# Optimization experiments

Hardware: AMD Instinct MI355X
Metric: run time of the kernel (lower is better)

## Reference

```python
import jax, jax.numpy as jnp
import numpy as np

B, IN, FS, S, H = 4096, 4096, 4096, 64, 512  # batch, input_size, first_size, shape_lstm, n_hidden
D = FS // S  # per-step feature for left/right (=64); up/down per-step feature = S (=64)


def _lstm_cell(x, h, c, Wih, Whh, bih, bhh):
    # standard torch LSTMCell gate order: i, f, g, o
    g = x @ Wih.T + bih + h @ Whh.T + bhh  # (B, 4H)
    i, f, gg, o = jnp.split(g, 4, axis=-1)
    c = jax.nn.sigmoid(f) * c + jax.nn.sigmoid(i) * jnp.tanh(gg)
    h = jax.nn.sigmoid(o) * jnp.tanh(c)
    return h, c


def setup_inputs() -> dict:
    key = jax.random.key(0)
    ks = jax.random.split(key, 20)
    def cell(k, d_in):
        k1, k2, k3, k4 = jax.random.split(k, 4)
        s = 1.0 / np.sqrt(H)
        return (jax.random.uniform(k1, (4 * H, d_in), jnp.float32, -s, s),
                jax.random.uniform(k2, (4 * H, H), jnp.float32, -s, s),
                jax.random.uniform(k3, (4 * H,), jnp.float32, -s, s),
                jax.random.uniform(k4, (4 * H,), jnp.float32, -s, s))
    Wih_l, Whh_l, bih_l, bhh_l = cell(ks[0], D)
    Wih_r, Whh_r, bih_r, bhh_r = cell(ks[1], D)
    Wih_d, Whh_d, bih_d, bhh_d = cell(ks[2], S)
    return {
        "x": jax.random.normal(ks[3], (B, IN), jnp.float32),
        "h0": jax.random.normal(ks[4], (4, B, H), jnp.float32),
        "c0": jax.random.normal(ks[5], (4, B, H), jnp.float32),
        "W1": jax.random.normal(ks[6], (FS, IN), jnp.float32) * (1.0 / np.sqrt(IN)),
        "b1": jnp.zeros((FS,), jnp.float32),
        "Wih_l": Wih_l, "Whh_l": Whh_l, "bih_l": bih_l, "bhh_l": bhh_l,
        "Wih_r": Wih_r, "Whh_r": Whh_r, "bih_r": bih_r, "bhh_r": bhh_r,
        "Wih_d": Wih_d, "Whh_d": Whh_d, "bih_d": bih_d, "bhh_d": bhh_d,
        "W3": jax.random.normal(ks[7], (10, 4 * H), jnp.float32) * (1.0 / np.sqrt(4 * H)),
        "b3": jnp.zeros((10,), jnp.float32),
    }


def reference(x, h0, c0, W1, b1, Wih_l, Whh_l, bih_l, bhh_l,
              Wih_r, Whh_r, bih_r, bhh_r, Wih_d, Whh_d, bih_d, bhh_d, W3, b3):
    feat = jax.nn.relu(x @ W1.T + b1)            # (B, FS); dropout=identity (eval)
    il = feat.reshape(B, S, D)
    x_left = jnp.transpose(il, (1, 0, 2))         # (S, B, D)
    x_right = x_left[::-1]
    x_up = jnp.transpose(il, (2, 0, 1))           # (D, B, S); loop uses first S steps
    x_down = x_up[::-1]

    def step(carry, xs):
        (hl, cl, hr, cr, hu, cu, hd, cd) = carry
        xl, xr, xu, xd = xs
        hl, cl = _lstm_cell(xl, hl, cl, Wih_l, Whh_l, bih_l, bhh_l)
        hr, cr = _lstm_cell(xr, hr, cr, Wih_r, Whh_r, bih_r, bhh_r)
        # original code uses the DOWN cell for both up and down directions
        hu, cu = _lstm_cell(xu, hu, cu, Wih_d, Whh_d, bih_d, bhh_d)
        hd, cd = _lstm_cell(xd, hd, cd, Wih_d, Whh_d, bih_d, bhh_d)
        return (hl, cl, hr, cr, hu, cu, hd, cd), None

    carry0 = (h0[0], c0[0], h0[1], c0[1], h0[2], c0[2], h0[3], c0[3])
    (hl, _, hr, _, hu, _, hd, _), _ = jax.lax.scan(
        step, carry0, (x_left[:S], x_right[:S], x_up[:S], x_down[:S]))
    out = jnp.concatenate([hl, hr, hu, hd], axis=1)  # (B, 4H)
    logits = out @ W3.T + b3
    return jax.nn.log_softmax(logits, axis=1)
```

## Files before the change

kernel.cpp:

```cpp
#include <hip/hip_runtime.h>
#include <cstddef>
#include <cstdint>

namespace {

constexpr int kB  = 4096;
constexpr int kIN = 4096;
constexpr int kFS = 4096;
constexpr int kS  = 64;
constexpr int kH  = 512;
constexpr int kNG = 2048;
constexpr int kKC = 576;

typedef __bf16 bf16_t;
typedef __bf16 bfrag  __attribute__((ext_vector_type(8)));
typedef __bf16 bf16v4 __attribute__((ext_vector_type(4)));
typedef float  f32x4  __attribute__((ext_vector_type(4)));

__device__ __forceinline__ void gload16(const void* g, void* l) {
  __builtin_amdgcn_global_load_lds(
      (const __attribute__((address_space(1))) void*)g,
      (__attribute__((address_space(3))) void*)l, 16, 0, 0);
}

__device__ __forceinline__ float sigf(float x) { return 1.0f / (1.0f + __expf(-x)); }
__device__ __forceinline__ float tanh_fast(float x) {
  float e = __expf(2.0f * x);
  return 1.0f - 2.0f / (e + 1.0f);
}

__device__ __forceinline__ f32x4 mfma16(bfrag a, bfrag b, f32x4 c) {
  return __builtin_amdgcn_mfma_f32_16x16x32_bf16(a, b, c, 0, 0, 0);
}


__global__ __launch_bounds__(256) void f2b4_kernel(const float* __restrict__ in,
                                                   bf16_t* __restrict__ out, int n4) {
  int i = blockIdx.x * 256 + threadIdx.x;
  if (i >= n4) return;
  float4 v = reinterpret_cast<const float4*>(in)[i];
  bf16v4 o = {(bf16_t)v.x, (bf16_t)v.y, (bf16_t)v.z, (bf16_t)v.w};
  *reinterpret_cast<bf16v4*>(out + (size_t)i * 4) = o;
}

__global__ __launch_bounds__(256) void pack_wcat_kernel(
    const float* __restrict__ Wih_l, const float* __restrict__ Whh_l,
    const float* __restrict__ Wih_r, const float* __restrict__ Whh_r,
    const float* __restrict__ Wih_d, const float* __restrict__ Whh_d,
    bf16_t* __restrict__ wcat) {
  int idx = blockIdx.x * 256 + threadIdx.x;
  if (idx >= 3 * kNG * kKC) return;
  int m = idx / (kNG * kKC);
  int rem = idx - m * (kNG * kKC);
  int rr = rem / kKC;
  int k  = rem - rr * kKC;
  int u = rr >> 2, g = rr & 3;
  int orow = g * kH + u;
  const float* Wih = (m == 0) ? Wih_l : (m == 1) ? Wih_r : Wih_d;
  const float* Whh = (m == 0) ? Whh_l : (m == 1) ? Whh_r : Whh_d;
  float v = (k < 64) ? Wih[(size_t)orow * 64 + k] : Whh[(size_t)orow * 512 + (k - 64)];
  wcat[idx] = (bf16_t)v;
}

__global__ __launch_bounds__(256) void pack_bias_kernel(
    const float* __restrict__ bih_l, const float* __restrict__ bhh_l,
    const float* __restrict__ bih_r, const float* __restrict__ bhh_r,
    const float* __restrict__ bih_d, const float* __restrict__ bhh_d,
    float* __restrict__ biasc) {
  int idx = blockIdx.x * 256 + threadIdx.x;
  if (idx >= 3 * kNG) return;
  int m = idx / kNG;
  int rr = idx - m * kNG;
  int u = rr >> 2, g = rr & 3;
  int orow = g * kH + u;
  const float* bi = (m == 0) ? bih_l : (m == 1) ? bih_r : bih_d;
  const float* bh = (m == 0) ? bhh_l : (m == 1) ? bhh_r : bhh_d;
  biasc[idx] = bi[orow] + bh[orow];
}

__global__ __launch_bounds__(256) void pack_hc_kernel(const float* __restrict__ h0,
                                                      const float* __restrict__ c0,
                                                      bf16_t* __restrict__ hbuf0,
                                                      float* __restrict__ cbuf, int n) {
  int i = blockIdx.x * 256 + threadIdx.x;
  if (i >= n) return;
  hbuf0[i] = (bf16_t)h0[i];
  cbuf[i]  = c0[i];
}

__global__ __launch_bounds__(256) void transpose64_kernel(const bf16_t* __restrict__ feat,
                                                          bf16_t* __restrict__ featT) {
  __shared__ bf16_t tile[64][65];
  const int b = blockIdx.x;
  const bf16_t* src = feat + (size_t)b * kFS;
  bf16_t* dst = featT + (size_t)b * kFS;
  for (int i = threadIdx.x; i < 4096; i += 256) tile[i >> 6][i & 63] = src[i];
  __syncthreads();
  for (int i = threadIdx.x; i < 4096; i += 256) dst[i] = tile[i & 63][i >> 6];
}


__global__ __launch_bounds__(256, 4) void gemm_feat_kernel(
    const bf16_t* __restrict__ X, const bf16_t* __restrict__ W,
    const float* __restrict__ b1, bf16_t* __restrict__ feat) {
  __shared__ bf16_t As[128 * 32];
  __shared__ bf16_t Bs[128 * 32];
  const int t = threadIdx.x;
  const int bid = blockIdx.x;
  const int widx = (bid & 7) * 128 + (bid >> 3);
  const int bm = widx & 31, bn = widx >> 5;
  const int w = t >> 6, l = t & 63;
  const int wm = (w >> 1) * 64, wn = (w & 1) * 64;
  const int sr = t >> 2;
  const int skS = ((t & 3) ^ ((t >> 3) & 3)) * 8;
  const int lr = l & 15;
  const int lkS = ((l >> 4) ^ ((l >> 1) & 3)) * 8;
  const int lrow4 = (l >> 4) * 4;

  f32x4 acc[4][4];
#pragma unroll
  for (int i = 0; i < 4; ++i)
#pragma unroll
    for (int j = 0; j < 4; ++j) acc[i][j] = (f32x4){0.f, 0.f, 0.f, 0.f};

  const bf16_t* ga = X + (size_t)(bm * 128 + sr) * kIN + skS;
  const bf16_t* gb = W + (size_t)(bn * 128 + sr) * kIN + skS;
  bf16_t* lA = As + w * 512;
  bf16_t* lB = Bs + w * 512;

  for (int kt = 0; kt < kIN / 32; ++kt) {
    gload16(ga, lA);
    gload16(ga + (size_t)64 * kIN, lA + 2048);
    gload16(gb, lB);
    gload16(gb + (size_t)64 * kIN, lB + 2048);
    ga += 32; gb += 32;
    __syncthreads();
    bfrag a[4], b[4];
#pragma unroll
    for (int mi = 0; mi < 4; ++mi)
      a[mi] = *reinterpret_cast<const bfrag*>(&As[(wm + mi * 16 + lr) * 32 + lkS]);
#pragma unroll
    for (int ni = 0; ni < 4; ++ni)
      b[ni] = *reinterpret_cast<const bfrag*>(&Bs[(wn + ni * 16 + lr) * 32 + lkS]);
#pragma unroll
    for (int mi = 0; mi < 4; ++mi)
#pragma unroll
      for (int ni = 0; ni < 4; ++ni)
        acc[mi][ni] = __builtin_amdgcn_mfma_f32_16x16x32_bf16(a[mi], b[ni], acc[mi][ni], 0, 0, 0);
    __syncthreads();
  }

#pragma unroll
  for (int ni = 0; ni < 4; ++ni) {
    const int col = bn * 128 + wn + ni * 16 + lr;
    const float bb = b1[col];
#pragma unroll
    for (int mi = 0; mi < 4; ++mi) {
#pragma unroll
      for (int r = 0; r < 4; ++r) {
        const int row = bm * 128 + wm + mi * 16 + lrow4 + r;
        float v = acc[mi][ni][r] + bb;
        feat[(size_t)row * kFS + col] = (bf16_t)fmaxf(v, 0.0f);
      }
    }
  }
}


__global__ __launch_bounds__(256, 2) void lstm_step128_kernel(
    const bf16_t* __restrict__ feat, const bf16_t* __restrict__ featT,
    const bf16_t* __restrict__ wcat, const float* __restrict__ biasc,
    const bf16_t* __restrict__ hin, bf16_t* __restrict__ hout,
    float* __restrict__ cbuf, int s) {
  extern __shared__ __align__(16) char smem[];

  const int t = threadIdx.x;
  const int l = t & 63, w = t >> 6;
  const int wm = (w >> 1) * 64, wn = (w & 1) * 64;
  const int lr = l & 15, lq = l >> 4;
  const int sx = lr & 7;
  const int srow = l >> 3;
  const int sslot = (l & 7) ^ srow;

  const int bid = blockIdx.x;
  const int widx = (bid & 7) * 256 + (bid >> 3);
  const int cell = widx >> 9;
  const int rwk = widx & 511;
  const int bm = rwk >> 4, bn = rwk & 15;

  const bf16_t* xsrc = (cell < 2) ? feat : featT;
  const int off = ((cell & 1) ? (63 - s) : s) * 64;
  const int mat = (cell < 2) ? cell : 2;
  const bf16_t* Wm = wcat + (size_t)mat * kNG * kKC;
  const bf16_t* hc = hin + (size_t)cell * kB * kH;

  auto stage = [&](int kt, int buf) {
    char* base = smem + buf * 32768;
#pragma unroll
    for (int j = 0; j < 4; ++j) {
      const int row0 = j * 32 + w * 8;
      bf16_t* dst = (bf16_t*)base + row0 * 64;
      const bf16_t* src = (kt == 0)
          ? xsrc + (size_t)(bm * 128 + row0 + srow) * kFS + off + sslot * 8
          : hc + (size_t)(bm * 128 + row0 + srow) * kH + (kt - 1) * 64 + sslot * 8;
      gload16(src, dst);
    }
#pragma unroll
    for (int j = 0; j < 4; ++j) {
      const int row0 = j * 32 + w * 8;
      bf16_t* dst = (bf16_t*)(base + 16384) + row0 * 64;
      const bf16_t* src =
          Wm + (size_t)(bn * 128 + row0 + srow) * kKC + kt * 64 + sslot * 8;
      gload16(src, dst);
    }
  };

  f32x4 acc[4][4];
#pragma unroll
  for (int i = 0; i < 4; ++i)
#pragma unroll
    for (int j = 0; j < 4; ++j) acc[i][j] = (f32x4){0.f, 0.f, 0.f, 0.f};

  stage(0, 0);
  asm volatile("s_waitcnt vmcnt(0)" ::: "memory");
  __builtin_amdgcn_sched_barrier(0);
  __builtin_amdgcn_s_barrier();

  for (int kt = 0; kt < 9; ++kt) {
    const int cur = kt & 1;
    if (kt < 8) stage(kt + 1, cur ^ 1);
    const bf16_t* As_ = (const bf16_t*)(smem + cur * 32768);
    const bf16_t* Bs_ = (const bf16_t*)(smem + cur * 32768 + 16384);
    bfrag a[8], b[8];
#pragma unroll
    for (int mi = 0; mi < 4; ++mi)
#pragma unroll
      for (int kk = 0; kk < 2; ++kk)
        a[mi * 2 + kk] = *reinterpret_cast<const bfrag*>(
            As_ + (wm + mi * 16 + lr) * 64 + (((kk * 4 + lq) ^ sx) * 8));
#pragma unroll
    for (int ni = 0; ni < 4; ++ni)
#pragma unroll
      for (int kk = 0; kk < 2; ++kk)
        b[ni * 2 + kk] = *reinterpret_cast<const bfrag*>(
            Bs_ + (wn + ni * 16 + lr) * 64 + (((kk * 4 + lq) ^ sx) * 8));
    __builtin_amdgcn_s_setprio(1);
#pragma unroll
    for (int kk = 0; kk < 2; ++kk)
#pragma unroll
      for (int mi = 0; mi < 4; ++mi)
#pragma unroll
        for (int ni = 0; ni < 4; ++ni)
          acc[mi][ni] = mfma16(a[mi * 2 + kk], b[ni * 2 + kk], acc[mi][ni]);
    __builtin_amdgcn_s_setprio(0);
    __builtin_amdgcn_sched_barrier(0);
    asm volatile("s_waitcnt vmcnt(0)" ::: "memory");
    __builtin_amdgcn_sched_barrier(0);
    __builtin_amdgcn_s_barrier();
  }

  float* Gw = (float*)(smem + 32768 + w * 4352);
  const float* biasn = biasc + mat * kNG + bn * 128 + wn;
  float bb[4];
#pragma unroll
  for (int n = 0; n < 4; ++n) bb[n] = biasn[n * 16 + lr];
  const int rowg0 = bm * 128 + wm;
  const int unit0 = bn * 32 + (w & 1) * 16;
#pragma unroll
  for (int mi = 0; mi < 4; ++mi) {
#pragma unroll
    for (int n = 0; n < 4; ++n)
#pragma unroll
      for (int j = 0; j < 4; ++j)
        Gw[(lq * 4 + j) * 68 + n * 16 + lr] = acc[mi][n][j] + bb[n];
#pragma unroll
    for (int it = 0; it < 4; ++it) {
      const int item = it * 64 + l;
      const int row = item >> 4;
      const int u = item & 15;
      const float4 g4 = *reinterpret_cast<const float4*>(&Gw[row * 68 + u * 4]);
      const float iv = sigf(g4.x);
      const float fv = sigf(g4.y);
      const float gv = tanh_fast(g4.z);
      const float ov = sigf(g4.w);
      const int grow = rowg0 + mi * 16 + row;
      const size_t cidx = ((size_t)cell * kB + grow) * kH + unit0 + u;
      const float cn = fv * cbuf[cidx] + iv * gv;
      cbuf[cidx] = cn;
      hout[cidx] = (bf16_t)(ov * tanh_fast(cn));
    }
  }
}


__global__ __launch_bounds__(256) void head_kernel(const bf16_t* __restrict__ hfin,
                                                   const float* __restrict__ W3,
                                                   const float* __restrict__ b3,
                                                   float* __restrict__ out) {
  const int b = blockIdx.x, t = threadIdx.x;
  const int l = t & 63, w = t >> 6;
  float acc[10];
#pragma unroll
  for (int j = 0; j < 10; ++j) acc[j] = 0.f;
  for (int k = t; k < 2048; k += 256) {
    const int cell = k >> 9, u = k & 511;
    const float hv = (float)hfin[((size_t)cell * kB + b) * kH + u];
#pragma unroll
    for (int j = 0; j < 10; ++j) acc[j] += hv * W3[j * 2048 + k];
  }
#pragma unroll
  for (int j = 0; j < 10; ++j)
#pragma unroll
    for (int o = 32; o > 0; o >>= 1) acc[j] += __shfl_down(acc[j], o, 64);
  __shared__ float wred[4][10];
  if (l == 0)
#pragma unroll
    for (int j = 0; j < 10; ++j) wred[w][j] = acc[j];
  __syncthreads();
  if (t == 0) {
    float logits[10];
#pragma unroll
    for (int j = 0; j < 10; ++j)
      logits[j] = wred[0][j] + wred[1][j] + wred[2][j] + wred[3][j] + b3[j];
    float mx = logits[0];
#pragma unroll
    for (int j = 1; j < 10; ++j) mx = fmaxf(mx, logits[j]);
    float se = 0.f;
#pragma unroll
    for (int j = 0; j < 10; ++j) se += expf(logits[j] - mx);
    const float lse = mx + logf(se);
#pragma unroll
    for (int j = 0; j < 10; ++j) out[(size_t)b * 10 + j] = logits[j] - lse;
  }
}

}

extern "C" void kernel_launch(void* const* d_in, const int* in_sizes, int n_in,
                              void* d_out, int out_size, void* d_ws, size_t ws_size,
                              hipStream_t stream) {
  const float* x     = (const float*)d_in[0];
  const float* h0    = (const float*)d_in[1];
  const float* c0    = (const float*)d_in[2];
  const float* W1    = (const float*)d_in[3];
  const float* b1    = (const float*)d_in[4];
  const float* Wih_l = (const float*)d_in[5];
  const float* Whh_l = (const float*)d_in[6];
  const float* bih_l = (const float*)d_in[7];
  const float* bhh_l = (const float*)d_in[8];
  const float* Wih_r = (const float*)d_in[9];
  const float* Whh_r = (const float*)d_in[10];
  const float* bih_r = (const float*)d_in[11];
  const float* bhh_r = (const float*)d_in[12];
  const float* Wih_d = (const float*)d_in[13];
  const float* Whh_d = (const float*)d_in[14];
  const float* bih_d = (const float*)d_in[15];
  const float* bhh_d = (const float*)d_in[16];
  const float* W3    = (const float*)d_in[17];
  const float* b3    = (const float*)d_in[18];
  float* out = (float*)d_out;

  char* p = (char*)d_ws;
  auto take = [&](size_t bytes) {
    char* r = p;
    p += (bytes + 255) & ~(size_t)255;
    return r;
  };
  bf16_t* xb    = (bf16_t*)take((size_t)kB * kIN * 2);
  bf16_t* w1b   = (bf16_t*)take((size_t)kFS * kIN * 2);
  bf16_t* feat  = (bf16_t*)take((size_t)kB * kFS * 2);
  bf16_t* wcat  = (bf16_t*)take((size_t)3 * kNG * kKC * 2);
  float*  biasc = (float*)take((size_t)3 * kNG * 4);
  float*  cbuf  = (float*)take((size_t)4 * kB * kH * 4);
  bf16_t* featT = xb;
  bf16_t* hbuf  = w1b;
  const size_t HSZ = (size_t)4 * kB * kH;

  (void)hipFuncSetAttribute(reinterpret_cast<const void*>(&lstm_step128_kernel),
                            hipFuncAttributeMaxDynamicSharedMemorySize, 65536);

  f2b4_kernel<<<(kB * kIN / 4) / 256, 256, 0, stream>>>(x, xb, kB * kIN / 4);
  f2b4_kernel<<<(kFS * kIN / 4) / 256, 256, 0, stream>>>(W1, w1b, kFS * kIN / 4);
  gemm_feat_kernel<<<dim3(1024), 256, 0, stream>>>(xb, w1b, b1, feat);
  transpose64_kernel<<<kB, 256, 0, stream>>>(feat, featT);
  pack_wcat_kernel<<<(3 * kNG * kKC + 255) / 256, 256, 0, stream>>>(
      Wih_l, Whh_l, Wih_r, Whh_r, Wih_d, Whh_d, wcat);
  pack_bias_kernel<<<(3 * kNG + 255) / 256, 256, 0, stream>>>(
      bih_l, bhh_l, bih_r, bhh_r, bih_d, bhh_d, biasc);
  pack_hc_kernel<<<(int)(HSZ / 256), 256, 0, stream>>>(h0, c0, hbuf, cbuf, (int)HSZ);

  for (int s = 0; s < 64; ++s) {
    lstm_step128_kernel<<<dim3(2048), 256, 65536, stream>>>(
        feat, featT, wcat, biasc,
        hbuf + (size_t)(s & 1) * HSZ, hbuf + (size_t)((s + 1) & 1) * HSZ, cbuf, s);
  }
  head_kernel<<<kB, 256, 0, stream>>>(hbuf, W3, b3, out);
}
```

Baseline: 4.118 ms.

## Enlarge LSTM step tiles, pre-swizzle weights into MFMA fragments loaded to registers

The per-step LSTM GEMM now uses 256x256 tiles with 512 threads (8 waves, 2x4), so there are 512 blocks instead of 2048. Weights are repacked offline into MFMA fragment order and loaded straight from global memory into registers with double buffering, which removes their LDS staging. The gate column order is rearranged so each wave holds i, f, g and o for the same units in its accumulators, letting the cell update run in registers without the LDS round trip. The cost is more registers per thread (32 accumulators plus two B fragment sets) and lower occupancy.

```diff
diff --git a/kernel.cpp b/kernel.cpp
--- a/kernel.cpp
+++ b/kernel.cpp
@@ -43,23 +43,31 @@
   *reinterpret_cast<bf16v4*>(out + (size_t)i * 4) = o;
 }
 
-__global__ __launch_bounds__(256) void pack_wcat_kernel(
+__global__ __launch_bounds__(256) void pack_wcat2_kernel(
     const float* __restrict__ Wih_l, const float* __restrict__ Whh_l,
     const float* __restrict__ Wih_r, const float* __restrict__ Whh_r,
     const float* __restrict__ Wih_d, const float* __restrict__ Whh_d,
-    bf16_t* __restrict__ wcat) {
+    bf16_t* __restrict__ wcat2) {
+  const int total = 3 * 128 * 9 * 2 * 64 * 8;
   int idx = blockIdx.x * 256 + threadIdx.x;
-  if (idx >= 3 * kNG * kKC) return;
-  int m = idx / (kNG * kKC);
-  int rem = idx - m * (kNG * kKC);
-  int rr = rem / kKC;
-  int k  = rem - rr * kKC;
-  int u = rr >> 2, g = rr & 3;
-  int orow = g * kH + u;
-  const float* Wih = (m == 0) ? Wih_l : (m == 1) ? Wih_r : Wih_d;
-  const float* Whh = (m == 0) ? Whh_l : (m == 1) ? Whh_r : Whh_d;
+  if (idx >= total) return;
+  int e  = idx & 7;
+  int l  = (idx >> 3) & 63;
+  int kk = (idx >> 9) & 1;
+  int r  = idx >> 10;
+  int kt = r % 9;
+  int matnb = r / 9;
+  int mat = matnb >> 7;
+  int nb  = matnb & 127;
+  const int c = nb * 16 + (l & 15);
+  const int g = (c >> 4) & 3;
+  const int u = (c >> 6) * 16 + (c & 15);
+  const int orow = g * kH + u;
+  const int k = kt * 64 + kk * 32 + (l >> 4) * 8 + e;
+  const float* Wih = (mat == 0) ? Wih_l : (mat == 1) ? Wih_r : Wih_d;
+  const float* Whh = (mat == 0) ? Whh_l : (mat == 1) ? Whh_r : Whh_d;
   float v = (k < 64) ? Wih[(size_t)orow * 64 + k] : Whh[(size_t)orow * 512 + (k - 64)];
-  wcat[idx] = (bf16_t)v;
+  wcat2[idx] = (bf16_t)v;
 }
 
 __global__ __launch_bounds__(256) void pack_bias_kernel(
@@ -69,12 +77,13 @@
     float* __restrict__ biasc) {
   int idx = blockIdx.x * 256 + threadIdx.x;
   if (idx >= 3 * kNG) return;
-  int m = idx / kNG;
-  int rr = idx - m * kNG;
-  int u = rr >> 2, g = rr & 3;
+  int mat = idx / kNG;
+  int c = idx - mat * kNG;
+  int g = (c >> 4) & 3;
+  int u = (c >> 6) * 16 + (c & 15);
   int orow = g * kH + u;
-  const float* bi = (m == 0) ? bih_l : (m == 1) ? bih_r : bih_d;
-  const float* bh = (m == 0) ? bhh_l : (m == 1) ? bhh_r : bhh_d;
+  const float* bi = (mat == 0) ? bih_l : (mat == 1) ? bih_r : bih_d;
+  const float* bh = (mat == 0) ? bhh_l : (mat == 1) ? bhh_r : bhh_d;
   biasc[idx] = bi[orow] + bh[orow];
 }
 
@@ -167,124 +176,138 @@
 }
 
 
-__global__ __launch_bounds__(256, 2) void lstm_step128_kernel(
+__global__ __launch_bounds__(512, 1) void lstm_step_kernel(
     const bf16_t* __restrict__ feat, const bf16_t* __restrict__ featT,
-    const bf16_t* __restrict__ wcat, const float* __restrict__ biasc,
+    const bf16_t* __restrict__ wcat2, const float* __restrict__ biasc,
     const bf16_t* __restrict__ hin, bf16_t* __restrict__ hout,
     float* __restrict__ cbuf, int s) {
   extern __shared__ __align__(16) char smem[];
 
   const int t = threadIdx.x;
   const int l = t & 63, w = t >> 6;
-  const int wm = (w >> 1) * 64, wn = (w & 1) * 64;
+  const int wr = w >> 2, wc = w & 3;
   const int lr = l & 15, lq = l >> 4;
   const int sx = lr & 7;
   const int srow = l >> 3;
-  const int sslot = (l & 7) ^ srow;
+  const int sslot = (l & 7) ^ (srow & 7);
 
   const int bid = blockIdx.x;
-  const int widx = (bid & 7) * 256 + (bid >> 3);
-  const int cell = widx >> 9;
-  const int rwk = widx & 511;
-  const int bm = rwk >> 4, bn = rwk & 15;
+  const int widx = (bid & 7) * 64 + (bid >> 3);
+  const int cell = widx >> 7;
+  const int rwk = widx & 127;
+  const int bm = rwk >> 3, bn = rwk & 7;
 
   const bf16_t* xsrc = (cell < 2) ? feat : featT;
   const int off = ((cell & 1) ? (63 - s) : s) * 64;
   const int mat = (cell < 2) ? cell : 2;
-  const bf16_t* Wm = wcat + (size_t)mat * kNG * kKC;
   const bf16_t* hc = hin + (size_t)cell * kB * kH;
 
-  auto stage = [&](int kt, int buf) {
-    char* base = smem + buf * 32768;
+  auto stageA = [&](int kt, int buf) {
+    bf16_t* base = (bf16_t*)(smem + buf * 32768);
 #pragma unroll
     for (int j = 0; j < 4; ++j) {
-      const int row0 = j * 32 + w * 8;
-      bf16_t* dst = (bf16_t*)base + row0 * 64;
+      const int row0 = j * 64 + w * 8;
+      bf16_t* dst = base + row0 * 64;
       const bf16_t* src = (kt == 0)
-          ? xsrc + (size_t)(bm * 128 + row0 + srow) * kFS + off + sslot * 8
-          : hc + (size_t)(bm * 128 + row0 + srow) * kH + (kt - 1) * 64 + sslot * 8;
-      gload16(src, dst);
-    }
-#pragma unroll
-    for (int j = 0; j < 4; ++j) {
-      const int row0 = j * 32 + w * 8;
-      bf16_t* dst = (bf16_t*)(base + 16384) + row0 * 64;
-      const bf16_t* src =
-          Wm + (size_t)(bn * 128 + row0 + srow) * kKC + kt * 64 + sslot * 8;
+          ? xsrc + (size_t)(bm * 256 + row0 + srow) * kFS + off + sslot * 8
+          : hc + (size_t)(bm * 256 + row0 + srow) * kH + (kt - 1) * 64 + sslot * 8;
       gload16(src, dst);
     }
   };
 
-  f32x4 acc[4][4];
-#pragma unroll
-  for (int i = 0; i < 4; ++i)
+  const size_t wb0 = ((size_t)mat * 128 + bn * 16 + wc * 4) * 9;
+  auto loadB = [&](int kt, bfrag (&d)[8]) {
+#pragma unroll
+    for (int nn = 0; nn < 4; ++nn)
+#pragma unroll
+      for (int kk = 0; kk < 2; ++kk)
+        d[nn * 2 + kk] = *reinterpret_cast<const bfrag*>(
+            wcat2 + (((wb0 + (size_t)nn * 9 + kt) * 2 + kk) << 9) + l * 8);
+  };
+
+  f32x4 acc[8][4];
+#pragma unroll
+  for (int i = 0; i < 8; ++i)
 #pragma unroll
     for (int j = 0; j < 4; ++j) acc[i][j] = (f32x4){0.f, 0.f, 0.f, 0.f};
 
-  stage(0, 0);
+  bfrag bA[8], bB[8];
+
+  stageA(0, 0);
+  loadB(0, bA);
   asm volatile("s_waitcnt vmcnt(0)" ::: "memory");
   __builtin_amdgcn_sched_barrier(0);
   __builtin_amdgcn_s_barrier();
 
+#pragma unroll
   for (int kt = 0; kt < 9; ++kt) {
     const int cur = kt & 1;
-    if (kt < 8) stage(kt + 1, cur ^ 1);
     const bf16_t* As_ = (const bf16_t*)(smem + cur * 32768);
-    const bf16_t* Bs_ = (const bf16_t*)(smem + cur * 32768 + 16384);
-    bfrag a[8], b[8];
+    bfrag (&bCur)[8] = (kt & 1) ? bB : bA;
+    bfrag (&bNxt)[8] = (kt & 1) ? bA : bB;
+
+    if (kt < 8) stageA(kt + 1, cur ^ 1);
+
+    bfrag a[8];
 #pragma unroll
     for (int mi = 0; mi < 4; ++mi)
 #pragma unroll
       for (int kk = 0; kk < 2; ++kk)
         a[mi * 2 + kk] = *reinterpret_cast<const bfrag*>(
-            As_ + (wm + mi * 16 + lr) * 64 + (((kk * 4 + lq) ^ sx) * 8));
-#pragma unroll
-    for (int ni = 0; ni < 4; ++ni)
+            As_ + (wr * 128 + mi * 16 + lr) * 64 + (((kk * 4 + lq) ^ sx) * 8));
+    __builtin_amdgcn_s_setprio(1);
+#pragma unroll
+    for (int kk = 0; kk < 2; ++kk)
+#pragma unroll
+      for (int mi = 0; mi < 4; ++mi)
+#pragma unroll
+        for (int nn = 0; nn < 4; ++nn)
+          acc[mi][nn] = mfma16(a[mi * 2 + kk], bCur[nn * 2 + kk], acc[mi][nn]);
+    __builtin_amdgcn_s_setprio(0);
+
+    if (kt < 8) loadB(kt + 1, bNxt);
+
+#pragma unroll
+    for (int mi = 0; mi < 4; ++mi)
 #pragma unroll
       for (int kk = 0; kk < 2; ++kk)
-        b[ni * 2 + kk] = *reinterpret_cast<const bfrag*>(
-            Bs_ + (wn + ni * 16 + lr) * 64 + (((kk * 4 + lq) ^ sx) * 8));
+        a[mi * 2 + kk] = *reinterpret_cast<const bfrag*>(
+            As_ + (wr * 128 + 64 + mi * 16 + lr) * 64 + (((kk * 4 + lq) ^ sx) * 8));
     __builtin_amdgcn_s_setprio(1);
 #pragma unroll
     for (int kk = 0; kk < 2; ++kk)
 #pragma unroll
       for (int mi = 0; mi < 4; ++mi)
 #pragma unroll
-        for (int ni = 0; ni < 4; ++ni)
-          acc[mi][ni] = mfma16(a[mi * 2 + kk], b[ni * 2 + kk], acc[mi][ni]);
+        for (int nn = 0; nn < 4; ++nn)
+          acc[4 + mi][nn] = mfma16(a[mi * 2 + kk], bCur[nn * 2 + kk], acc[4 + mi][nn]);
     __builtin_amdgcn_s_setprio(0);
     __builtin_amdgcn_sched_barrier(0);
-    asm volatile("s_waitcnt vmcnt(0)" ::: "memory");
-    __builtin_amdgcn_sched_barrier(0);
-    __builtin_amdgcn_s_barrier();
-  }
-
-  float* Gw = (float*)(smem + 32768 + w * 4352);
-  const float* biasn = biasc + mat * kNG + bn * 128 + wn;
-  float bb[4];
-#pragma unroll
-  for (int n = 0; n < 4; ++n) bb[n] = biasn[n * 16 + lr];
-  const int rowg0 = bm * 128 + wm;
-  const int unit0 = bn * 32 + (w & 1) * 16;
-#pragma unroll
-  for (int mi = 0; mi < 4; ++mi) {
-#pragma unroll
-    for (int n = 0; n < 4; ++n)
-#pragma unroll
-      for (int j = 0; j < 4; ++j)
-        Gw[(lq * 4 + j) * 68 + n * 16 + lr] = acc[mi][n][j] + bb[n];
-#pragma unroll
-    for (int it = 0; it < 4; ++it) {
-      const int item = it * 64 + l;
-      const int row = item >> 4;
-      const int u = item & 15;
-      const float4 g4 = *reinterpret_cast<const float4*>(&Gw[row * 68 + u * 4]);
-      const float iv = sigf(g4.x);
-      const float fv = sigf(g4.y);
-      const float gv = tanh_fast(g4.z);
-      const float ov = sigf(g4.w);
-      const int grow = rowg0 + mi * 16 + row;
-      const size_t cidx = ((size_t)cell * kB + grow) * kH + unit0 + u;
+
+    if (kt < 8) {
+      asm volatile("s_waitcnt vmcnt(8)" ::: "memory");
+      __builtin_amdgcn_sched_barrier(0);
+      __builtin_amdgcn_s_barrier();
+    }
+  }
+
+  const float* biasn = biasc + mat * kNG + bn * 256 + wc * 64;
+  const float bb0 = biasn[0 * 16 + lr];
+  const float bb1 = biasn[1 * 16 + lr];
+  const float bb2 = biasn[2 * 16 + lr];
+  const float bb3 = biasn[3 * 16 + lr];
+  const int u = (bn * 4 + wc) * 16 + lr;
+  const int row0 = bm * 256 + wr * 128 + lq * 4;
+#pragma unroll
+  for (int mi = 0; mi < 8; ++mi) {
+#pragma unroll
+    for (int j = 0; j < 4; ++j) {
+      const float iv = sigf(acc[mi][0][j] + bb0);
+      const float fv = sigf(acc[mi][1][j] + bb1);
+      const float gv = tanh_fast(acc[mi][2][j] + bb2);
+      const float ov = sigf(acc[mi][3][j] + bb3);
+      const int row = row0 + mi * 16 + j;
+      const size_t cidx = ((size_t)cell * kB + row) * kH + u;
       const float cn = fv * cbuf[cidx] + iv * gv;
       cbuf[cidx] = cn;
       hout[cidx] = (bf16_t)(ov * tanh_fast(cn));
@@ -369,29 +392,32 @@
   bf16_t* xb    = (bf16_t*)take((size_t)kB * kIN * 2);
   bf16_t* w1b   = (bf16_t*)take((size_t)kFS * kIN * 2);
   bf16_t* feat  = (bf16_t*)take((size_t)kB * kFS * 2);
-  bf16_t* wcat  = (bf16_t*)take((size_t)3 * kNG * kKC * 2);
+  bf16_t* wcat2 = (bf16_t*)take((size_t)3 * 128 * 9 * 2 * 64 * 8 * 2);
   float*  biasc = (float*)take((size_t)3 * kNG * 4);
   float*  cbuf  = (float*)take((size_t)4 * kB * kH * 4);
   bf16_t* featT = xb;
   bf16_t* hbuf  = w1b;
   const size_t HSZ = (size_t)4 * kB * kH;
 
-  (void)hipFuncSetAttribute(reinterpret_cast<const void*>(&lstm_step128_kernel),
+  (void)hipFuncSetAttribute(reinterpret_cast<const void*>(&lstm_step_kernel),
                             hipFuncAttributeMaxDynamicSharedMemorySize, 65536);
 
   f2b4_kernel<<<(kB * kIN / 4) / 256, 256, 0, stream>>>(x, xb, kB * kIN / 4);
   f2b4_kernel<<<(kFS * kIN / 4) / 256, 256, 0, stream>>>(W1, w1b, kFS * kIN / 4);
   gemm_feat_kernel<<<dim3(1024), 256, 0, stream>>>(xb, w1b, b1, feat);
   transpose64_kernel<<<kB, 256, 0, stream>>>(feat, featT);
-  pack_wcat_kernel<<<(3 * kNG * kKC + 255) / 256, 256, 0, stream>>>(
-      Wih_l, Whh_l, Wih_r, Whh_r, Wih_d, Whh_d, wcat);
+  {
+    const int total = 3 * 128 * 9 * 2 * 64 * 8;
+    pack_wcat2_kernel<<<(total + 255) / 256, 256, 0, stream>>>(
+        Wih_l, Whh_l, Wih_r, Whh_r, Wih_d, Whh_d, wcat2);
+  }
   pack_bias_kernel<<<(3 * kNG + 255) / 256, 256, 0, stream>>>(
       bih_l, bhh_l, bih_r, bhh_r, bih_d, bhh_d, biasc);
   pack_hc_kernel<<<(int)(HSZ / 256), 256, 0, stream>>>(h0, c0, hbuf, cbuf, (int)HSZ);
 
   for (int s = 0; s < 64; ++s) {
-    lstm_step128_kernel<<<dim3(2048), 256, 65536, stream>>>(
-        feat, featT, wcat, biasc,
+    lstm_step_kernel<<<dim3(512), 512, 65536, stream>>>(
+        feat, featT, wcat2, biasc,
         hbuf + (size_t)(s & 1) * HSZ, hbuf + (size_t)((s + 1) & 1) * HSZ, cbuf, s);
   }
   head_kernel<<<kB, 256, 0, stream>>>(hbuf, W3, b3, out);
```

Result: faster. 3.834 ms, median of 2 (-6.9%).
